# Kernel optimization log

Hardware: AMD Instinct MI355X
Metric: run time of the kernel (lower is better)

Reference implementation:

```python
import jax, jax.numpy as jnp
import numpy as np


def _apply_1q_batched(state, gate, q):
    # state: (B,2,2,2,2) complex; gate: (B,2,2) complex; acts on qubit q
    state = jnp.moveaxis(state, q + 1, -1)
    state = jnp.einsum('bij,b...j->b...i', gate, state)
    return jnp.moveaxis(state, -1, q + 1)


def _apply_cnot(state, c, t):
    # flip target bit where control bit == 1
    s0, s1 = jnp.split(state, 2, axis=c + 1)
    s1 = jnp.flip(s1, axis=t + 1)
    return jnp.concatenate([s0, s1], axis=c + 1)


def _quantum_features(angles, params):
    # angles: (B,4) RY rotation angles; params: (4,) RZ angles
    B = angles.shape[0]
    state = jnp.zeros((B, 16), jnp.complex64).at[:, 0].set(1.0).reshape(B, 2, 2, 2, 2)
    # RY(x_i) on each wire (batched angle per sample)
    for q in range(4):
        th = 0.5 * angles[:, q]
        c, s = jnp.cos(th), jnp.sin(th)
        gate = jnp.stack([jnp.stack([c, -s], -1), jnp.stack([s, c], -1)], -2).astype(jnp.complex64)
        state = _apply_1q_batched(state, gate, q)
    # RZ(params[i]) on wire i followed by CNOT(i, (i+1)%4), interleaved as in source
    pc = params.astype(jnp.complex64)
    for q in range(4):
        ph = jnp.exp(jnp.array([-0.5j, 0.5j], jnp.complex64) * pc[q])
        shp = [1, 1, 1, 1, 1]
        shp[q + 1] = 2
        state = state * ph.reshape(shp)
        state = _apply_cnot(state, q, (q + 1) % 4)
    probs = state.real ** 2 + state.imag ** 2  # (B,2,2,2,2)
    feats = []
    for q in range(4):
        axes = tuple(a for a in range(1, 5) if a != q + 1)
        p = probs.sum(axes)  # (B,2)
        feats.append(p[:, 0] - p[:, 1])  # <Z_q>
    return jnp.stack(feats, -1)  # (B,4)


def _deconv2x2(x, w, b):
    # PyTorch ConvTranspose2d with kernel=stride=2, padding=0 (non-overlapping)
    # x: (B,Ci,H,W), w: (Ci,Co,2,2), b: (Co,)
    B, Ci, H, W = x.shape
    Co = w.shape[1]
    y = jnp.einsum('bchw,codk->bohdwk', x, w).reshape(B, Co, 2 * H, 2 * W)
    return y + b[None, :, None, None]


def setup_inputs() -> dict:
    key = jax.random.key(0)
    ks = jax.random.split(key, 10)
    B = 16384
    return {
        'x': jax.random.uniform(ks[0], (B, 1, 28, 28), jnp.float32),
        'var_params': jax.random.normal(ks[1], (4,), jnp.float32),
        'w_lat': jax.random.normal(ks[2], (224, 4), jnp.float32) * 0.3,
        'b_lat': jax.random.normal(ks[3], (224,), jnp.float32) * 0.05,
        'w_fc': jax.random.normal(ks[4], (392, 224), jnp.float32) * 0.05,
        'b_fc': jax.random.normal(ks[5], (392,), jnp.float32) * 0.05,
        'w_d1': jax.random.normal(ks[6], (8, 4, 2, 2), jnp.float32) * 0.2,
        'b_d1': jax.random.normal(ks[7], (4,), jnp.float32) * 0.05,
        'w_d2': jax.random.normal(ks[8], (4, 1, 2, 2), jnp.float32) * 0.2,
        'b_d2': jax.random.normal(ks[9], (1,), jnp.float32) * 0.05,
    }


def reference(x, var_params, w_lat, b_lat, w_fc, b_fc, w_d1, b_d1, w_d2, b_d2):
    # quadrant means -> 4 angles per sample
    quad = jnp.stack([
        x[:, 0, :14, :14].mean((1, 2)),
        x[:, 0, :14, 14:].mean((1, 2)),
        x[:, 0, 14:, :14].mean((1, 2)),
        x[:, 0, 14:, 14:].mean((1, 2)),
    ], axis=1)  # (B,4)
    qf = _quantum_features(quad, var_params)  # (B,4)
    latent = jax.nn.relu(qf @ w_lat.T + b_lat)  # (B,224)
    h = jax.nn.relu(latent @ w_fc.T + b_fc)  # (B,392)
    h = h.reshape(-1, 8, 7, 7)
    h = jax.nn.relu(_deconv2x2(h, w_d1, b_d1))  # (B,4,14,14)
    out = jax.nn.sigmoid(_deconv2x2(h, w_d2, b_d2))  # (B,1,28,28)
    return out
```

## Files before the change

kernel.cpp:

```cpp
#include <hip/hip_runtime.h>
#include <math.h>

#define G 16
#define HS 396
#define LSTR 232

typedef __attribute__((ext_vector_type(8))) __bf16 bf16x8;
typedef __attribute__((ext_vector_type(4))) float f32x4;
typedef __attribute__((ext_vector_type(2))) float f32x2;

__global__ void wconv_kernel(const float* __restrict__ w_fc, __bf16* __restrict__ wb) {
  int tile = blockIdx.x;
  int kt   = blockIdx.y;
  int lane = threadIdx.x;
  int n  = tile * 16 + (lane & 15);
  int k0 = kt * 32 + (lane >> 4) * 8;
  bf16x8 v;
  if (n < 392) {
    const float* src = w_fc + (size_t)n * 224 + k0;
    float4 f0 = *(const float4*)(src);
    float4 f1 = *(const float4*)(src + 4);
    v[0] = (__bf16)f0.x; v[1] = (__bf16)f0.y; v[2] = (__bf16)f0.z; v[3] = (__bf16)f0.w;
    v[4] = (__bf16)f1.x; v[5] = (__bf16)f1.y; v[6] = (__bf16)f1.z; v[7] = (__bf16)f1.w;
  } else {
    #pragma unroll
    for (int j = 0; j < 8; ++j) v[j] = (__bf16)0.f;
  }
  *(bf16x8*)(wb + ((size_t)(tile * 7 + kt) * 64 + lane) * 8) = v;
}

__global__ __launch_bounds__(512, 8) void fused_kernel(
    const float* __restrict__ x, const float* __restrict__ params,
    const __bf16* __restrict__ wb,
    const float* __restrict__ w_lat, const float* __restrict__ b_lat,
    const float* __restrict__ b_fc,
    const float* __restrict__ w_d1, const float* __restrict__ b_d1,
    const float* __restrict__ w_d2, const float* __restrict__ b_d2,
    float* __restrict__ out, int B)
{
  __shared__ __align__(16) __bf16 latb[G * LSTR];
  __shared__ __align__(16) float hbuf[G * HS];
  __shared__ __align__(16) float qfs[G * 4];
  __shared__ float wd1[128];
  __shared__ float wd2[16];
  __shared__ float bd1[4];
  const int t = threadIdx.x;
  const int wv = t >> 6;
  const int lane = t & 63;
  const int s0g = blockIdx.x * G;
  if (s0g >= B) return;

  if (t < 128) wd1[t] = w_d1[t];
  else if (t < 144) wd2[t - 128] = w_d2[t - 128];
  else if (t < 148) bd1[t - 144] = b_d1[t - 144];

  {
    const float* xb = x + (size_t)(s0g + wv * 2) * 784;
    f32x4 vb[2][4];
    #pragma unroll
    for (int smp = 0; smp < 2; ++smp)
      #pragma unroll
      for (int it = 0; it < 4; ++it) {
        int i4 = lane + it * 64;
        if (i4 < 196)
          vb[smp][it] = __builtin_nontemporal_load((const f32x4*)(xb + smp * 784 + i4 * 4));
        else
          vb[smp][it] = (f32x4){0.f, 0.f, 0.f, 0.f};
      }
    float acc[2][4];
    #pragma unroll
    for (int i = 0; i < 2; ++i)
      #pragma unroll
      for (int q = 0; q < 4; ++q) acc[i][q] = 0.f;
    #pragma unroll
    for (int it = 0; it < 4; ++it) {
      int i4 = lane + it * 64;
      int base = i4 * 4;
      int r = base / 28;
      int cb = base - r * 28;
      float bt = (r >= 14) ? 1.f : 0.f;
      float tp = 1.f - bt;
      float w0[4], w1[4], w2[4], w3[4];
      #pragma unroll
      for (int e = 0; e < 4; ++e) {
        float lf = ((cb + e) < 14) ? 1.f : 0.f;
        float rf = 1.f - lf;
        w0[e] = tp * lf; w1[e] = tp * rf; w2[e] = bt * lf; w3[e] = bt * rf;
      }
      #pragma unroll
      for (int smp = 0; smp < 2; ++smp) {
        f32x4 v = vb[smp][it];
        #pragma unroll
        for (int e = 0; e < 4; ++e) {
          acc[smp][0] = fmaf(v[e], w0[e], acc[smp][0]);
          acc[smp][1] = fmaf(v[e], w1[e], acc[smp][1]);
          acc[smp][2] = fmaf(v[e], w2[e], acc[smp][2]);
          acc[smp][3] = fmaf(v[e], w3[e], acc[smp][3]);
        }
      }
    }
    #pragma unroll
    for (int smp = 0; smp < 2; ++smp)
      #pragma unroll
      for (int q = 0; q < 4; ++q)
        #pragma unroll
        for (int o = 32; o > 0; o >>= 1)
          acc[smp][q] += __shfl_down(acc[smp][q], o, 64);
    if (lane == 0) {
      const float inv = 1.f / 196.f;
      #pragma unroll
      for (int smp = 0; smp < 2; ++smp) {
        float4 o;
        o.x = acc[smp][0] * inv; o.y = acc[smp][1] * inv;
        o.z = acc[smp][2] * inv; o.w = acc[smp][3] * inv;
        *(float4*)(qfs + (wv * 2 + smp) * 4) = o;
      }
    }
  }

  {
    const int sub = lane >> 4;
    const int i   = lane & 15;
    const int s   = wv * 2 + (sub & 1);
    float4 mn = *(const float4*)(qfs + s * 4);
    float c_[4], s_[4];
    c_[0] = __cosf(0.5f * mn.x); s_[0] = __sinf(0.5f * mn.x);
    c_[1] = __cosf(0.5f * mn.y); s_[1] = __sinf(0.5f * mn.y);
    c_[2] = __cosf(0.5f * mn.z); s_[2] = __sinf(0.5f * mn.z);
    c_[3] = __cosf(0.5f * mn.w); s_[3] = __sinf(0.5f * mn.w);
    float re = (((i >> 3) & 1) ? s_[0] : c_[0]) * (((i >> 2) & 1) ? s_[1] : c_[1])
             * (((i >> 1) & 1) ? s_[2] : c_[2]) * ((i & 1) ? s_[3] : c_[3]);
    float im = 0.f;
    #pragma unroll
    for (int q = 0; q < 4; ++q) {
      float hp = 0.5f * params[q];
      float sp = __sinf(hp), cp = __cosf(hp);
      int qb = 3 - q;
      float sg = ((i >> qb) & 1) ? sp : -sp;
      float r0 = re, i0 = im;
      re = r0 * cp - i0 * sg;
      im = r0 * sg + i0 * cp;
      int cm = 1 << qb;
      int tm = 1 << (3 - ((q + 1) & 3));
      int srcI = (i & cm) ? (i ^ tm) : i;
      int srcLane = (lane & ~15) | srcI;
      re = __shfl(re, srcLane, 64);
      im = __shfl(im, srcLane, 64);
    }
    float p = re * re + im * im;
    float z[4];
    #pragma unroll
    for (int q = 0; q < 4; ++q) {
      int qb = 3 - q;
      float v = ((i >> qb) & 1) ? -p : p;
      v += __shfl_xor(v, 1, 16);
      v += __shfl_xor(v, 2, 16);
      v += __shfl_xor(v, 4, 16);
      v += __shfl_xor(v, 8, 16);
      z[q] = v;
    }
    if (sub < 2 && i < 4) {
      float zv = (i == 0) ? z[0] : (i == 1) ? z[1] : (i == 2) ? z[2] : z[3];
      qfs[s * 4 + i] = zv;
    }
  }

  #pragma unroll
  for (int sl = 0; sl < 2; ++sl) {
    int s = wv * 2 + sl;
    float4 q4 = *(const float4*)(qfs + s * 4);
    for (int j = lane; j < 224; j += 64) {
      float4 w = *(const float4*)(w_lat + j * 4);
      float a = b_lat[j];
      a = fmaf(q4.x, w.x, a);
      a = fmaf(q4.y, w.y, a);
      a = fmaf(q4.z, w.z, a);
      a = fmaf(q4.w, w.w, a);
      latb[s * LSTR + j] = (__bf16)fmaxf(a, 0.f);
    }
  }
  __syncthreads();

  {
    const int m = lane & 15;
    const int kq = lane >> 4;
    const __bf16* arow = latb + m * LSTR + kq * 8;
    for (int tile = wv; tile < 25; tile += 8) {
      f32x4 acc = {0.f, 0.f, 0.f, 0.f};
      const bf16x8* bp = (const bf16x8*)(wb + ((size_t)(tile * 7) * 64 + lane) * 8);
      #pragma unroll
      for (int kt = 0; kt < 7; ++kt) {
        bf16x8 a = *(const bf16x8*)(arow + kt * 32);
        bf16x8 b = bp[kt * 64];
        acc = __builtin_amdgcn_mfma_f32_16x16x32_bf16(a, b, acc, 0, 0, 0);
      }
      int j = tile * 16 + m;
      if (j < 392) {
        float bf = b_fc[j];
        #pragma unroll
        for (int r = 0; r < 4; ++r)
          hbuf[(kq * 4 + r) * HS + j] = fmaxf(acc[r] + bf, 0.f);
      }
    }
  }
  __syncthreads();

  const float bd2v = b_d2[0];
  for (int v = t; v < G * 196; v += 512) {
    int s = v / 196;
    int p = v - s * 196;
    int Y = p / 14;
    int X = p - Y * 14;
    int y = Y >> 1, ey = Y & 1, xx = X >> 1, ex = X & 1;
    const float* hs = hbuf + s * HS + y * 7 + xx;
    float hv[8];
    #pragma unroll
    for (int ci = 0; ci < 8; ++ci) hv[ci] = hs[ci * 49];
    float o1[4];
    #pragma unroll
    for (int co = 0; co < 4; ++co) {
      float a = bd1[co];
      #pragma unroll
      for (int ci = 0; ci < 8; ++ci)
        a = fmaf(hv[ci], wd1[ci * 16 + co * 4 + ey * 2 + ex], a);
      o1[co] = fmaxf(a, 0.f);
    }
    size_t basep = (size_t)(s0g + s) * 784;
    #pragma unroll
    for (int dy = 0; dy < 2; ++dy) {
      float v0 = bd2v, v1 = bd2v;
      #pragma unroll
      for (int co = 0; co < 4; ++co) {
        v0 = fmaf(o1[co], wd2[co * 4 + dy * 2 + 0], v0);
        v1 = fmaf(o1[co], wd2[co * 4 + dy * 2 + 1], v1);
      }
      f32x2 o;
      o[0] = 1.f / (1.f + __expf(-v0));
      o[1] = 1.f / (1.f + __expf(-v1));
      __builtin_nontemporal_store(o, (f32x2*)(out + basep + (size_t)(2 * Y + dy) * 28 + 2 * X));
    }
  }
}

extern "C" void kernel_launch(void* const* d_in, const int* in_sizes, int n_in,
                              void* d_out, int out_size, void* d_ws, size_t ws_size,
                              hipStream_t stream) {
  const float* x          = (const float*)d_in[0];
  const float* var_params = (const float*)d_in[1];
  const float* w_lat      = (const float*)d_in[2];
  const float* b_lat      = (const float*)d_in[3];
  const float* w_fc       = (const float*)d_in[4];
  const float* b_fc       = (const float*)d_in[5];
  const float* w_d1       = (const float*)d_in[6];
  const float* b_d1       = (const float*)d_in[7];
  const float* w_d2       = (const float*)d_in[8];
  const float* b_d2       = (const float*)d_in[9];
  float* out = (float*)d_out;

  __bf16* wb = (__bf16*)d_ws;

  int B = in_sizes[0] / 784;
  wconv_kernel<<<dim3(25, 7), 64, 0, stream>>>(w_fc, wb);
  fused_kernel<<<(B + G - 1) / G, 512, 0, stream>>>(
      x, var_params, wb, w_lat, b_lat, b_fc, w_d1, b_d1, w_d2, b_d2, out, B);
}
```

Before: 137.4 us.

## Drop weight pre-conversion kernel and store FC activations as bf16 in LDS

Removes the separate wconv launch that packed w_fc into bf16 MFMA layout; each block now loads fp32 w_fc rows from global memory and converts them to bf16 in registers before each MFMA. The hidden buffer in shared memory is also stored as bf16 instead of fp32, halving its LDS footprint, which may allow more blocks per CU. This trades a kernel launch for doubled weight read traffic and extra conversions in every block, and adds precision loss on the hidden activations.

```diff
diff --git a/kernel.cpp b/kernel.cpp
--- a/kernel.cpp
+++ b/kernel.cpp
@@ -2,36 +2,16 @@
 #include <math.h>
 
 #define G 16
-#define HS 396
+#define HS2 400
 #define LSTR 232
 
 typedef __attribute__((ext_vector_type(8))) __bf16 bf16x8;
 typedef __attribute__((ext_vector_type(4))) float f32x4;
 typedef __attribute__((ext_vector_type(2))) float f32x2;
 
-__global__ void wconv_kernel(const float* __restrict__ w_fc, __bf16* __restrict__ wb) {
-  int tile = blockIdx.x;
-  int kt   = blockIdx.y;
-  int lane = threadIdx.x;
-  int n  = tile * 16 + (lane & 15);
-  int k0 = kt * 32 + (lane >> 4) * 8;
-  bf16x8 v;
-  if (n < 392) {
-    const float* src = w_fc + (size_t)n * 224 + k0;
-    float4 f0 = *(const float4*)(src);
-    float4 f1 = *(const float4*)(src + 4);
-    v[0] = (__bf16)f0.x; v[1] = (__bf16)f0.y; v[2] = (__bf16)f0.z; v[3] = (__bf16)f0.w;
-    v[4] = (__bf16)f1.x; v[5] = (__bf16)f1.y; v[6] = (__bf16)f1.z; v[7] = (__bf16)f1.w;
-  } else {
-    #pragma unroll
-    for (int j = 0; j < 8; ++j) v[j] = (__bf16)0.f;
-  }
-  *(bf16x8*)(wb + ((size_t)(tile * 7 + kt) * 64 + lane) * 8) = v;
-}
-
 __global__ __launch_bounds__(512, 8) void fused_kernel(
     const float* __restrict__ x, const float* __restrict__ params,
-    const __bf16* __restrict__ wb,
+    const float* __restrict__ w_fc,
     const float* __restrict__ w_lat, const float* __restrict__ b_lat,
     const float* __restrict__ b_fc,
     const float* __restrict__ w_d1, const float* __restrict__ b_d1,
@@ -39,7 +19,7 @@
     float* __restrict__ out, int B)
 {
   __shared__ __align__(16) __bf16 latb[G * LSTR];
-  __shared__ __align__(16) float hbuf[G * HS];
+  __shared__ __align__(16) __bf16 hbuf[G * HS2];
   __shared__ __align__(16) float qfs[G * 4];
   __shared__ float wd1[128];
   __shared__ float wd2[16];
@@ -186,12 +166,26 @@
     const int kq = lane >> 4;
     const __bf16* arow = latb + m * LSTR + kq * 8;
     for (int tile = wv; tile < 25; tile += 8) {
+      int n = tile * 16 + m;
+      bool valid = n < 392;
+      const float* wr = w_fc + (size_t)n * 224 + kq * 8;
       f32x4 acc = {0.f, 0.f, 0.f, 0.f};
-      const bf16x8* bp = (const bf16x8*)(wb + ((size_t)(tile * 7) * 64 + lane) * 8);
       #pragma unroll
       for (int kt = 0; kt < 7; ++kt) {
+        f32x4 blo, bhi;
+        if (valid) {
+          blo = *(const f32x4*)(wr + kt * 32);
+          bhi = *(const f32x4*)(wr + kt * 32 + 4);
+        } else {
+          blo = (f32x4){0.f, 0.f, 0.f, 0.f};
+          bhi = (f32x4){0.f, 0.f, 0.f, 0.f};
+        }
+        bf16x8 b;
+        b[0] = (__bf16)blo[0]; b[1] = (__bf16)blo[1];
+        b[2] = (__bf16)blo[2]; b[3] = (__bf16)blo[3];
+        b[4] = (__bf16)bhi[0]; b[5] = (__bf16)bhi[1];
+        b[6] = (__bf16)bhi[2]; b[7] = (__bf16)bhi[3];
         bf16x8 a = *(const bf16x8*)(arow + kt * 32);
-        bf16x8 b = bp[kt * 64];
         acc = __builtin_amdgcn_mfma_f32_16x16x32_bf16(a, b, acc, 0, 0, 0);
       }
       int j = tile * 16 + m;
@@ -199,7 +193,7 @@
         float bf = b_fc[j];
         #pragma unroll
         for (int r = 0; r < 4; ++r)
-          hbuf[(kq * 4 + r) * HS + j] = fmaxf(acc[r] + bf, 0.f);
+          hbuf[(kq * 4 + r) * HS2 + j] = (__bf16)fmaxf(acc[r] + bf, 0.f);
       }
     }
   }
@@ -212,10 +206,10 @@
     int Y = p / 14;
     int X = p - Y * 14;
     int y = Y >> 1, ey = Y & 1, xx = X >> 1, ex = X & 1;
-    const float* hs = hbuf + s * HS + y * 7 + xx;
+    const __bf16* hs = hbuf + s * HS2 + y * 7 + xx;
     float hv[8];
     #pragma unroll
-    for (int ci = 0; ci < 8; ++ci) hv[ci] = hs[ci * 49];
+    for (int ci = 0; ci < 8; ++ci) hv[ci] = (float)hs[ci * 49];
     float o1[4];
     #pragma unroll
     for (int co = 0; co < 4; ++co) {
@@ -256,11 +250,9 @@
   const float* w_d2       = (const float*)d_in[8];
   const float* b_d2       = (const float*)d_in[9];
   float* out = (float*)d_out;
-
-  __bf16* wb = (__bf16*)d_ws;
+  (void)d_ws; (void)ws_size;
 
   int B = in_sizes[0] / 784;
-  wconv_kernel<<<dim3(25, 7), 64, 0, stream>>>(w_fc, wb);
   fused_kernel<<<(B + G - 1) / G, 512, 0, stream>>>(
-      x, var_params, wb, w_lat, b_lat, b_fc, w_d1, b_d1, w_d2, b_d2, out, B);
+      x, var_params, w_fc, w_lat, b_lat, b_fc, w_d1, b_d1, w_d2, b_d2, out, B);
 }
```

Result: slower. 158.7 us (+15.5%).
